# Kernel tuning notes

Measured on AMD Instinct MI355X. Metric: run time of the kernel, lower is better.

## Reference

```python
import jax, jax.numpy as jnp
import numpy as np


def setup_inputs() -> dict:
    key = jax.random.key(0)
    ks = jax.random.split(key, 9)
    n, L, H, H2 = 1024, 256, 512, 256
    return {
        "lstms0": jax.random.normal(ks[0], (n, L), jnp.float32),
        "lstms1": jax.random.normal(ks[1], (n, L), jnp.float32),
        "W_foh": jax.random.normal(ks[2], (2 * L, H), jnp.float32) * 0.05,
        "W_fom": jax.random.normal(ks[3], (2 * L, H), jnp.float32) * 0.05,
        "catBias": jax.random.normal(ks[4], (1, 2 * H), jnp.float32) * 0.05,
        "hid2Layer": jax.random.normal(ks[5], (2 * H, H2), jnp.float32) * 0.05,
        "hid2Bias": jax.random.normal(ks[6], (1, H2), jnp.float32) * 0.05,
        "outLayer": jax.random.normal(ks[7], (H2, 1), jnp.float32) * 0.05,
        "outBias": jax.random.normal(ks[8], (1, 1), jnp.float32) * 0.05,
    }


def reference(lstms0, lstms1, W_foh, W_fom, catBias, hid2Layer, hid2Bias, outLayer, outBias):
    act = jnp.tanh
    H = W_foh.shape[1]
    # per-token concatenated BiLSTM state: [n, 2L]
    x = jnp.concatenate([lstms0, lstms1], axis=-1)
    headfov = x @ W_foh  # [n, H]
    modfov = x @ W_fom   # [n, H]
    # activation(concat(head_i, mod_j) + catBias) is elementwise, so it splits:
    ah = act(headfov + catBias[0, :H])  # [n, H]
    am = act(modfov + catBias[0, H:])   # [n, H]
    # concat(ah_i, am_j) @ hid2Layer == ah_i @ W_top + am_j @ W_bot
    A = ah @ hid2Layer[:H]  # [n, H2]
    B = am @ hid2Layer[H:]  # [n, H2]
    # pairwise hidden: [n_head, n_mod, H2]
    Z = act(A[:, None, :] + B[None, :, :] + hid2Bias[0])
    scores = jnp.einsum("ijh,h->ij", Z, outLayer[:, 0]) + outBias[0, 0]
    return scores  # [n, n], scores[i, j] = score(head=i, mod=j)
```

## Files before the change

### kernel.cpp

```cpp
#include <hip/hip_runtime.h>
#include <hip/hip_bf16.h>

typedef short s16x8 __attribute__((ext_vector_type(8)));
typedef float f32x4 __attribute__((ext_vector_type(4)));

#define LOG2E_2 2.8853900817779268f

__device__ __forceinline__ float fexp2(float x){ return __builtin_amdgcn_exp2f(x); }
__device__ __forceinline__ float frcp (float x){ return __builtin_amdgcn_rcpf(x); }
__device__ __forceinline__ float ftanh(float v){
    return 1.0f - 2.0f * frcp(1.0f + fexp2(LOG2E_2 * v));
}
__device__ __forceinline__ unsigned short f2bf(float v){
    __hip_bfloat16 h = __float2bfloat16(v);
    return __builtin_bit_cast(unsigned short, h);
}
__device__ __forceinline__ float bf2f(unsigned short u){
    return __bfloat162float(__builtin_bit_cast(__hip_bfloat16, u));
}
__device__ __forceinline__ f32x4 mfma32(s16x8 a, s16x8 b, f32x4 c){
    return __builtin_amdgcn_mfma_f32_16x16x32_bf16(a, b, c, 0, 0, 0);
}

__global__ __launch_bounds__(256) void prep_all(
    const float* __restrict__ l0, const float* __restrict__ l1,
    const float* __restrict__ Wfoh, const float* __restrict__ Wfom,
    const float* __restrict__ W2,
    unsigned short* __restrict__ xhi, unsigned short* __restrict__ xlo,
    unsigned short* __restrict__ w1hi, unsigned short* __restrict__ w1lo,
    unsigned short* __restrict__ w2hi, unsigned short* __restrict__ w2lo)
{
    __shared__ float F[32][33];
    const int t = threadIdx.x;
    const int bid = blockIdx.x;

    if (bid < 512) {
        int idx = (bid * 256 + t) * 4;
        int r = idx >> 9, c = idx & 511;
        float4 v = (c < 256) ? *(const float4*)(l0 + r*256 + c)
                             : *(const float4*)(l1 + r*256 + (c - 256));
        ushort4 h, l;
        h.x = f2bf(v.x); l.x = f2bf(v.x - bf2f(h.x));
        h.y = f2bf(v.y); l.y = f2bf(v.y - bf2f(h.y));
        h.z = f2bf(v.z); l.z = f2bf(v.z - bf2f(h.z));
        h.w = f2bf(v.w); l.w = f2bf(v.w - bf2f(h.w));
        *(ushort4*)(xhi + idx) = h;
        *(ushort4*)(xlo + idx) = l;
        return;
    }

    const float* srcA; const float* srcB;
    int splitN, lda, K, k0, n0;
    unsigned short *dhi, *dlo;
    if (bid < 1024) {
        int b = bid - 512;
        k0 = (b & 15) * 32; n0 = (b >> 4) * 32;
        srcA = Wfoh; srcB = Wfom; splitN = 512; lda = 512; K = 512;
        dhi = w1hi; dlo = w1lo;
    } else {
        int b = bid - 1024;
        k0 = (b & 31) * 32; n0 = (b >> 5) * 32;
        srcA = W2; srcB = W2; splitN = 1 << 30; lda = 256; K = 1024;
        dhi = w2hi; dlo = w2lo;
    }
    {
        int kk = t >> 3, n4 = (t & 7) * 4;
        int n = n0 + n4;
        const float* s = (n < splitN) ? (srcA + (k0+kk)*lda + n)
                                      : (srcB + (k0+kk)*lda + (n - splitN));
        float4 v = *(const float4*)s;
        F[kk][n4+0] = v.x; F[kk][n4+1] = v.y; F[kk][n4+2] = v.z; F[kk][n4+3] = v.w;
    }
    __syncthreads();
    {
        int nn = t >> 3, k4 = (t & 7) * 4;
        ushort4 h, l;
        float v0 = F[k4+0][nn]; h.x = f2bf(v0); l.x = f2bf(v0 - bf2f(h.x));
        float v1 = F[k4+1][nn]; h.y = f2bf(v1); l.y = f2bf(v1 - bf2f(h.y));
        float v2 = F[k4+2][nn]; h.z = f2bf(v2); l.z = f2bf(v2 - bf2f(h.z));
        float v3 = F[k4+3][nn]; h.w = f2bf(v3); l.w = f2bf(v3 - bf2f(h.w));
        *(ushort4*)(dhi + (n0+nn)*K + k0 + k4) = h;
        *(ushort4*)(dlo + (n0+nn)*K + k0 + k4) = l;
    }
}

__global__ __launch_bounds__(256) void k1_mfma(
    const unsigned short* __restrict__ xhi, const unsigned short* __restrict__ xlo,
    const unsigned short* __restrict__ whi, const unsigned short* __restrict__ wlo,
    const float* __restrict__ cb,
    unsigned short* __restrict__ hvhi, unsigned short* __restrict__ hvlo)
{
    __shared__ unsigned short Ah[64][40], Al[64][40], Bh[32][40], Bl[32][40];
    const int t = threadIdx.x;
    const int r0 = blockIdx.y * 64, c0 = blockIdx.x * 32;
    const int w = t >> 6, lane = t & 63;
    const int m = lane & 15, quad = lane >> 4;

    const int arow = t >> 2, aseg = t & 3;
    const int brow = (t & 127) >> 2, bseg = t & 3;
    const bool doB = (t < 128);

    f32x4 acc0 = {0,0,0,0}, acc1 = {0,0,0,0};

    const unsigned short* pAh = xhi + (r0+arow)*512 + aseg*8;
    const unsigned short* pAl = xlo + (r0+arow)*512 + aseg*8;
    const unsigned short* pBh = whi + (c0+brow)*512 + bseg*8;
    const unsigned short* pBl = wlo + (c0+brow)*512 + bseg*8;

    uint4 pah = *(const uint4*)pAh;
    uint4 pal = *(const uint4*)pAl;
    uint4 pbh = {}, pbl = {};
    if (doB) { pbh = *(const uint4*)pBh; pbl = *(const uint4*)pBl; }

    for (int c = 0; c < 16; ++c) {
        __syncthreads();
        *(uint4*)&Ah[arow][aseg*8] = pah;
        *(uint4*)&Al[arow][aseg*8] = pal;
        if (doB) {
            *(uint4*)&Bh[brow][bseg*8] = pbh;
            *(uint4*)&Bl[brow][bseg*8] = pbl;
        }
        __syncthreads();
        if (c + 1 < 16) {
            int k0 = (c+1) * 32;
            pah = *(const uint4*)(pAh + k0);
            pal = *(const uint4*)(pAl + k0);
            if (doB) {
                pbh = *(const uint4*)(pBh + k0);
                pbl = *(const uint4*)(pBl + k0);
            }
        }
        {
            const int ko = quad*8;
            s16x8 ah  = *(const s16x8*)&Ah[w*16 + m][ko];
            s16x8 al  = *(const s16x8*)&Al[w*16 + m][ko];
            s16x8 b0h = *(const s16x8*)&Bh[m][ko];
            s16x8 b0l = *(const s16x8*)&Bl[m][ko];
            s16x8 b1h = *(const s16x8*)&Bh[16 + m][ko];
            s16x8 b1l = *(const s16x8*)&Bl[16 + m][ko];
            acc0 = mfma32(ah, b0h, acc0);
            acc0 = mfma32(ah, b0l, acc0);
            acc0 = mfma32(al, b0h, acc0);
            acc1 = mfma32(ah, b1h, acc1);
            acc1 = mfma32(ah, b1l, acc1);
            acc1 = mfma32(al, b1h, acc1);
        }
    }

    #pragma unroll
    for (int nt = 0; nt < 2; ++nt) {
        f32x4 a = nt ? acc1 : acc0;
        const int col = c0 + nt*16 + m;
        const float bias = cb[col];
        #pragma unroll
        for (int reg = 0; reg < 4; ++reg) {
            const int row = r0 + w*16 + quad*4 + reg;
            float v = ftanh(a[reg] + bias);
            unsigned short h = f2bf(v);
            unsigned short l = f2bf(v - bf2f(h));
            hvhi[row*1024 + col] = h;
            hvlo[row*1024 + col] = l;
        }
    }
}

__global__ __launch_bounds__(256) void k2_mfma(
    const unsigned short* __restrict__ hvhi, const unsigned short* __restrict__ hvlo,
    const unsigned short* __restrict__ w2hi, const unsigned short* __restrict__ w2lo,
    const float* __restrict__ h2b, float* __restrict__ P)
{
    __shared__ unsigned short Ah[64][40], Al[64][40], Bh[32][40], Bl[32][40];
    const int t = threadIdx.x;
    const int r0 = blockIdx.y * 64, c0 = blockIdx.x * 32;
    const int half = (c0 >= 256) ? 1 : 0;
    const int ho = half * 512;
    const int nw = c0 & 255;
    const int w = t >> 6, lane = t & 63;
    const int m = lane & 15, quad = lane >> 4;

    const int arow = t >> 2, aseg = t & 3;
    const int brow = (t & 127) >> 2, bseg = t & 3;
    const bool doB = (t < 128);

    f32x4 acc0 = {0,0,0,0}, acc1 = {0,0,0,0};

    const unsigned short* pAh = hvhi + (r0+arow)*1024 + ho + aseg*8;
    const unsigned short* pAl = hvlo + (r0+arow)*1024 + ho + aseg*8;
    const unsigned short* pBh = w2hi + (nw+brow)*1024 + ho + bseg*8;
    const unsigned short* pBl = w2lo + (nw+brow)*1024 + ho + bseg*8;

    uint4 pah = *(const uint4*)pAh;
    uint4 pal = *(const uint4*)pAl;
    uint4 pbh = {}, pbl = {};
    if (doB) { pbh = *(const uint4*)pBh; pbl = *(const uint4*)pBl; }

    for (int c = 0; c < 16; ++c) {
        __syncthreads();
        *(uint4*)&Ah[arow][aseg*8] = pah;
        *(uint4*)&Al[arow][aseg*8] = pal;
        if (doB) {
            *(uint4*)&Bh[brow][bseg*8] = pbh;
            *(uint4*)&Bl[brow][bseg*8] = pbl;
        }
        __syncthreads();
        if (c + 1 < 16) {
            int k0 = (c+1) * 32;
            pah = *(const uint4*)(pAh + k0);
            pal = *(const uint4*)(pAl + k0);
            if (doB) {
                pbh = *(const uint4*)(pBh + k0);
                pbl = *(const uint4*)(pBl + k0);
            }
        }
        {
            const int ko = quad*8;
            s16x8 ah  = *(const s16x8*)&Ah[w*16 + m][ko];
            s16x8 al  = *(const s16x8*)&Al[w*16 + m][ko];
            s16x8 b0h = *(const s16x8*)&Bh[m][ko];
            s16x8 b0l = *(const s16x8*)&Bl[m][ko];
            s16x8 b1h = *(const s16x8*)&Bh[16 + m][ko];
            s16x8 b1l = *(const s16x8*)&Bl[16 + m][ko];
            acc0 = mfma32(ah, b0h, acc0);
            acc0 = mfma32(ah, b0l, acc0);
            acc0 = mfma32(al, b0h, acc0);
            acc1 = mfma32(ah, b1h, acc1);
            acc1 = mfma32(ah, b1l, acc1);
            acc1 = mfma32(al, b1h, acc1);
        }
    }

    #pragma unroll
    for (int nt = 0; nt < 2; ++nt) {
        f32x4 a = nt ? acc1 : acc0;
        const int col = c0 + nt*16 + m;
        const float bias = half ? 0.0f : h2b[col];
        #pragma unroll
        for (int reg = 0; reg < 4; ++reg) {
            const int row = r0 + w*16 + quad*4 + reg;
            P[row*512 + col] = fexp2((a[reg] + bias) * LOG2E_2);
        }
    }
}

__global__ __launch_bounds__(256) void k3_pairwise(
    const float* __restrict__ P, const float* __restrict__ w,
    const float* __restrict__ ob, float* __restrict__ out)
{
    __shared__ float As[64][68];
    __shared__ float Bs[32][68];
    __shared__ float wls[256];
    const int tid = threadIdx.x;
    const int tx = tid & 15;
    const int ty = tid >> 4;
    const int i0 = blockIdx.y * 64, j0 = blockIdx.x * 32;

    wls[tid] = w[tid];

    const int ar = tid >> 2, ac = (tid & 3) * 16;
    const int br = tid >> 3, bc = (tid & 7) * 8;

    const float* pA = P + (i0 + ar) * 512 + ac;
    const float* pB = P + (j0 + br) * 512 + 256 + bc;

    float acc[4][2] = {};
    float4 ra[4], rb[2];
    #pragma unroll
    for (int k = 0; k < 4; ++k) ra[k] = *(const float4*)(pA + k*4);
    #pragma unroll
    for (int k = 0; k < 2; ++k) rb[k] = *(const float4*)(pB + k*4);

    for (int c = 0; c < 4; ++c) {
        __syncthreads();
        #pragma unroll
        for (int k = 0; k < 4; ++k) *(float4*)&As[ar][ac + k*4] = ra[k];
        #pragma unroll
        for (int k = 0; k < 2; ++k) *(float4*)&Bs[br][bc + k*4] = rb[k];
        __syncthreads();
        if (c + 1 < 4) {
            int off = (c + 1) * 64;
            #pragma unroll
            for (int k = 0; k < 4; ++k) ra[k] = *(const float4*)(pA + off + k*4);
            #pragma unroll
            for (int k = 0; k < 2; ++k) rb[k] = *(const float4*)(pB + off + k*4);
        }

        #pragma unroll 2
        for (int hh = 0; hh < 64; hh += 4) {
            float4 wv = *(const float4*)&wls[c*64 + hh];
            float4 av[4];
            #pragma unroll
            for (int r = 0; r < 4; ++r) av[r] = *(const float4*)&As[ty*4 + r][hh];
            float4 bv[2];
            #pragma unroll
            for (int q = 0; q < 2; ++q) bv[q] = *(const float4*)&Bs[tx + 16*q][hh];
            #pragma unroll
            for (int r = 0; r < 4; ++r)
                #pragma unroll
                for (int q = 0; q < 2; ++q) {
                    float u0 = fmaf(av[r].x, bv[q].x, 1.0f);
                    float u1 = fmaf(av[r].y, bv[q].y, 1.0f);
                    float u2 = fmaf(av[r].z, bv[q].z, 1.0f);
                    float u3 = fmaf(av[r].w, bv[q].w, 1.0f);
                    float d01 = u0 * u1;
                    float d23 = u2 * u3;
                    float p01 = fmaf(wv.x, u1, wv.y * u0);
                    float p23 = fmaf(wv.z, u3, wv.w * u2);
                    float num = fmaf(p01, d23, p23 * d01);
                    acc[r][q] = fmaf(num, frcp(d01 * d23), acc[r][q]);
                }
        }
    }

    float sumw = 0.0f;
    #pragma unroll
    for (int h = 0; h < 256; h += 4) {
        float4 wv = *(const float4*)&wls[h];
        sumw += (wv.x + wv.y) + (wv.z + wv.w);
    }
    const float base = ob[0] + sumw;
    #pragma unroll
    for (int r = 0; r < 4; ++r) {
        const int row = i0 + ty*4 + r;
        out[row*1024 + j0 + tx]      = base - 2.0f * acc[r][0];
        out[row*1024 + j0 + tx + 16] = base - 2.0f * acc[r][1];
    }
}

extern "C" void kernel_launch(void* const* d_in, const int* in_sizes, int n_in,
                              void* d_out, int out_size, void* d_ws, size_t ws_size,
                              hipStream_t stream) {
    const float* l0   = (const float*)d_in[0];
    const float* l1   = (const float*)d_in[1];
    const float* Wfoh = (const float*)d_in[2];
    const float* Wfom = (const float*)d_in[3];
    const float* cb   = (const float*)d_in[4];
    const float* W2   = (const float*)d_in[5];
    const float* h2b  = (const float*)d_in[6];
    const float* w    = (const float*)d_in[7];
    const float* ob   = (const float*)d_in[8];
    float* out = (float*)d_out;

    unsigned short* hv_hi  = (unsigned short*)d_ws;
    unsigned short* hv_lo  = hv_hi + 1024*1024;
    float*          P      = (float*)(hv_lo + 1024*1024);
    unsigned short* xs_hi  = (unsigned short*)(P + 1024*512);
    unsigned short* xs_lo  = xs_hi + 1024*512;
    unsigned short* w1t_hi = xs_lo + 1024*512;
    unsigned short* w1t_lo = w1t_hi + 1024*512;
    unsigned short* w2t_hi = w1t_lo + 1024*512;
    unsigned short* w2t_lo = w2t_hi + 256*1024;

    prep_all<<<1280, 256, 0, stream>>>(l0, l1, Wfoh, Wfom, W2,
                                       xs_hi, xs_lo, w1t_hi, w1t_lo, w2t_hi, w2t_lo);
    k1_mfma<<<dim3(32,16), 256, 0, stream>>>(xs_hi, xs_lo, w1t_hi, w1t_lo, cb, hv_hi, hv_lo);
    k2_mfma<<<dim3(16,16), 256, 0, stream>>>(hv_hi, hv_lo, w2t_hi, w2t_lo, h2b, P);
    k3_pairwise<<<dim3(32,16), 256, 0, stream>>>(P, w, ob, out);
}
```

Before: 129.1 us.

## Double-buffer LDS tiles in GEMM kernels and shrink pairwise tile to 32x32

```diff
diff --git a/kernel.cpp b/kernel.cpp
--- a/kernel.cpp
+++ b/kernel.cpp
@@ -90,7 +90,7 @@
     const float* __restrict__ cb,
     unsigned short* __restrict__ hvhi, unsigned short* __restrict__ hvlo)
 {
-    __shared__ unsigned short Ah[64][40], Al[64][40], Bh[32][40], Bl[32][40];
+    __shared__ unsigned short Ah[2][64][40], Al[2][64][40], Bh[2][32][40], Bl[2][32][40];
     const int t = threadIdx.x;
     const int r0 = blockIdx.y * 64, c0 = blockIdx.x * 32;
     const int w = t >> 6, lane = t & 63;
@@ -112,38 +112,50 @@
     uint4 pbh = {}, pbl = {};
     if (doB) { pbh = *(const uint4*)pBh; pbl = *(const uint4*)pBl; }
 
+    *(uint4*)&Ah[0][arow][aseg*8] = pah;
+    *(uint4*)&Al[0][arow][aseg*8] = pal;
+    if (doB) {
+        *(uint4*)&Bh[0][brow][bseg*8] = pbh;
+        *(uint4*)&Bl[0][brow][bseg*8] = pbl;
+    }
+    pah = *(const uint4*)(pAh + 32);
+    pal = *(const uint4*)(pAl + 32);
+    if (doB) { pbh = *(const uint4*)(pBh + 32); pbl = *(const uint4*)(pBl + 32); }
+    __syncthreads();
+
+    #pragma unroll 2
     for (int c = 0; c < 16; ++c) {
-        __syncthreads();
-        *(uint4*)&Ah[arow][aseg*8] = pah;
-        *(uint4*)&Al[arow][aseg*8] = pal;
-        if (doB) {
-            *(uint4*)&Bh[brow][bseg*8] = pbh;
-            *(uint4*)&Bl[brow][bseg*8] = pbl;
-        }
-        __syncthreads();
-        if (c + 1 < 16) {
-            int k0 = (c+1) * 32;
-            pah = *(const uint4*)(pAh + k0);
-            pal = *(const uint4*)(pAl + k0);
-            if (doB) {
-                pbh = *(const uint4*)(pBh + k0);
-                pbl = *(const uint4*)(pBl + k0);
-            }
-        }
+        const int buf = c & 1;
         {
             const int ko = quad*8;
-            s16x8 ah  = *(const s16x8*)&Ah[w*16 + m][ko];
-            s16x8 al  = *(const s16x8*)&Al[w*16 + m][ko];
-            s16x8 b0h = *(const s16x8*)&Bh[m][ko];
-            s16x8 b0l = *(const s16x8*)&Bl[m][ko];
-            s16x8 b1h = *(const s16x8*)&Bh[16 + m][ko];
-            s16x8 b1l = *(const s16x8*)&Bl[16 + m][ko];
+            s16x8 ah  = *(const s16x8*)&Ah[buf][w*16 + m][ko];
+            s16x8 al  = *(const s16x8*)&Al[buf][w*16 + m][ko];
+            s16x8 b0h = *(const s16x8*)&Bh[buf][m][ko];
+            s16x8 b0l = *(const s16x8*)&Bl[buf][m][ko];
+            s16x8 b1h = *(const s16x8*)&Bh[buf][16 + m][ko];
+            s16x8 b1l = *(const s16x8*)&Bl[buf][16 + m][ko];
             acc0 = mfma32(ah, b0h, acc0);
             acc0 = mfma32(ah, b0l, acc0);
             acc0 = mfma32(al, b0h, acc0);
             acc1 = mfma32(ah, b1h, acc1);
             acc1 = mfma32(ah, b1l, acc1);
             acc1 = mfma32(al, b1h, acc1);
+        }
+        if (c + 1 < 16) {
+            const int nb = buf ^ 1;
+            *(uint4*)&Ah[nb][arow][aseg*8] = pah;
+            *(uint4*)&Al[nb][arow][aseg*8] = pal;
+            if (doB) {
+                *(uint4*)&Bh[nb][brow][bseg*8] = pbh;
+                *(uint4*)&Bl[nb][brow][bseg*8] = pbl;
+            }
+            if (c + 2 < 16) {
+                const int k0 = (c+2) * 32;
+                pah = *(const uint4*)(pAh + k0);
+                pal = *(const uint4*)(pAl + k0);
+                if (doB) { pbh = *(const uint4*)(pBh + k0); pbl = *(const uint4*)(pBl + k0); }
+            }
+            __syncthreads();
         }
     }
 
@@ -169,7 +181,7 @@
     const unsigned short* __restrict__ w2hi, const unsigned short* __restrict__ w2lo,
     const float* __restrict__ h2b, float* __restrict__ P)
 {
-    __shared__ unsigned short Ah[64][40], Al[64][40], Bh[32][40], Bl[32][40];
+    __shared__ unsigned short Ah[2][64][40], Al[2][64][40], Bh[2][32][40], Bl[2][32][40];
     const int t = threadIdx.x;
     const int r0 = blockIdx.y * 64, c0 = blockIdx.x * 32;
     const int half = (c0 >= 256) ? 1 : 0;
@@ -194,38 +206,50 @@
     uint4 pbh = {}, pbl = {};
     if (doB) { pbh = *(const uint4*)pBh; pbl = *(const uint4*)pBl; }
 
+    *(uint4*)&Ah[0][arow][aseg*8] = pah;
+    *(uint4*)&Al[0][arow][aseg*8] = pal;
+    if (doB) {
+        *(uint4*)&Bh[0][brow][bseg*8] = pbh;
+        *(uint4*)&Bl[0][brow][bseg*8] = pbl;
+    }
+    pah = *(const uint4*)(pAh + 32);
+    pal = *(const uint4*)(pAl + 32);
+    if (doB) { pbh = *(const uint4*)(pBh + 32); pbl = *(const uint4*)(pBl + 32); }
+    __syncthreads();
+
+    #pragma unroll 2
     for (int c = 0; c < 16; ++c) {
-        __syncthreads();
-        *(uint4*)&Ah[arow][aseg*8] = pah;
-        *(uint4*)&Al[arow][aseg*8] = pal;
-        if (doB) {
-            *(uint4*)&Bh[brow][bseg*8] = pbh;
-            *(uint4*)&Bl[brow][bseg*8] = pbl;
-        }
-        __syncthreads();
-        if (c + 1 < 16) {
-            int k0 = (c+1) * 32;
-            pah = *(const uint4*)(pAh + k0);
-            pal = *(const uint4*)(pAl + k0);
-            if (doB) {
-                pbh = *(const uint4*)(pBh + k0);
-                pbl = *(const uint4*)(pBl + k0);
-            }
-        }
+        const int buf = c & 1;
         {
             const int ko = quad*8;
-            s16x8 ah  = *(const s16x8*)&Ah[w*16 + m][ko];
-            s16x8 al  = *(const s16x8*)&Al[w*16 + m][ko];
-            s16x8 b0h = *(const s16x8*)&Bh[m][ko];
-            s16x8 b0l = *(const s16x8*)&Bl[m][ko];
-            s16x8 b1h = *(const s16x8*)&Bh[16 + m][ko];
-            s16x8 b1l = *(const s16x8*)&Bl[16 + m][ko];
+            s16x8 ah  = *(const s16x8*)&Ah[buf][w*16 + m][ko];
+            s16x8 al  = *(const s16x8*)&Al[buf][w*16 + m][ko];
+            s16x8 b0h = *(const s16x8*)&Bh[buf][m][ko];
+            s16x8 b0l = *(const s16x8*)&Bl[buf][m][ko];
+            s16x8 b1h = *(const s16x8*)&Bh[buf][16 + m][ko];
+            s16x8 b1l = *(const s16x8*)&Bl[buf][16 + m][ko];
             acc0 = mfma32(ah, b0h, acc0);
             acc0 = mfma32(ah, b0l, acc0);
             acc0 = mfma32(al, b0h, acc0);
             acc1 = mfma32(ah, b1h, acc1);
             acc1 = mfma32(ah, b1l, acc1);
             acc1 = mfma32(al, b1h, acc1);
+        }
+        if (c + 1 < 16) {
+            const int nb = buf ^ 1;
+            *(uint4*)&Ah[nb][arow][aseg*8] = pah;
+            *(uint4*)&Al[nb][arow][aseg*8] = pal;
+            if (doB) {
+                *(uint4*)&Bh[nb][brow][bseg*8] = pbh;
+                *(uint4*)&Bl[nb][brow][bseg*8] = pbl;
+            }
+            if (c + 2 < 16) {
+                const int k0 = (c+2) * 32;
+                pah = *(const uint4*)(pAh + k0);
+                pal = *(const uint4*)(pAl + k0);
+                if (doB) { pbh = *(const uint4*)(pBh + k0); pbl = *(const uint4*)(pBl + k0); }
+            }
+            __syncthreads();
         }
     }
 
@@ -246,55 +270,51 @@
     const float* __restrict__ P, const float* __restrict__ w,
     const float* __restrict__ ob, float* __restrict__ out)
 {
-    __shared__ float As[64][68];
-    __shared__ float Bs[32][68];
+    __shared__ float As[2][32][68];
+    __shared__ float Bs[2][32][68];
     __shared__ float wls[256];
     const int tid = threadIdx.x;
     const int tx = tid & 15;
     const int ty = tid >> 4;
-    const int i0 = blockIdx.y * 64, j0 = blockIdx.x * 32;
+    const int i0 = blockIdx.y * 32, j0 = blockIdx.x * 32;
 
     wls[tid] = w[tid];
 
-    const int ar = tid >> 2, ac = (tid & 3) * 16;
-    const int br = tid >> 3, bc = (tid & 7) * 8;
+    const int ar = tid >> 3, ac = (tid & 7) * 8;
 
     const float* pA = P + (i0 + ar) * 512 + ac;
-    const float* pB = P + (j0 + br) * 512 + 256 + bc;
-
-    float acc[4][2] = {};
-    float4 ra[4], rb[2];
-    #pragma unroll
-    for (int k = 0; k < 4; ++k) ra[k] = *(const float4*)(pA + k*4);
-    #pragma unroll
-    for (int k = 0; k < 2; ++k) rb[k] = *(const float4*)(pB + k*4);
-
+    const float* pB = P + (j0 + ar) * 512 + 256 + ac;
+
+    float4 ra0 = *(const float4*)(pA);
+    float4 ra1 = *(const float4*)(pA + 4);
+    float4 rb0 = *(const float4*)(pB);
+    float4 rb1 = *(const float4*)(pB + 4);
+
+    *(float4*)&As[0][ar][ac]   = ra0;
+    *(float4*)&As[0][ar][ac+4] = ra1;
+    *(float4*)&Bs[0][ar][ac]   = rb0;
+    *(float4*)&Bs[0][ar][ac+4] = rb1;
+    ra0 = *(const float4*)(pA + 64);
+    ra1 = *(const float4*)(pA + 68);
+    rb0 = *(const float4*)(pB + 64);
+    rb1 = *(const float4*)(pB + 68);
+    __syncthreads();
+
+    float acc[2][2] = {};
+
+    #pragma unroll 2
     for (int c = 0; c < 4; ++c) {
-        __syncthreads();
-        #pragma unroll
-        for (int k = 0; k < 4; ++k) *(float4*)&As[ar][ac + k*4] = ra[k];
-        #pragma unroll
-        for (int k = 0; k < 2; ++k) *(float4*)&Bs[br][bc + k*4] = rb[k];
-        __syncthreads();
-        if (c + 1 < 4) {
-            int off = (c + 1) * 64;
-            #pragma unroll
-            for (int k = 0; k < 4; ++k) ra[k] = *(const float4*)(pA + off + k*4);
-            #pragma unroll
-            for (int k = 0; k < 2; ++k) rb[k] = *(const float4*)(pB + off + k*4);
-        }
-
-        #pragma unroll 2
+        const int buf = c & 1;
+        #pragma unroll 4
         for (int hh = 0; hh < 64; hh += 4) {
             float4 wv = *(const float4*)&wls[c*64 + hh];
-            float4 av[4];
+            float4 av[2], bv[2];
+            av[0] = *(const float4*)&As[buf][ty][hh];
+            av[1] = *(const float4*)&As[buf][ty+16][hh];
+            bv[0] = *(const float4*)&Bs[buf][tx][hh];
+            bv[1] = *(const float4*)&Bs[buf][tx+16][hh];
             #pragma unroll
-            for (int r = 0; r < 4; ++r) av[r] = *(const float4*)&As[ty*4 + r][hh];
-            float4 bv[2];
-            #pragma unroll
-            for (int q = 0; q < 2; ++q) bv[q] = *(const float4*)&Bs[tx + 16*q][hh];
-            #pragma unroll
-            for (int r = 0; r < 4; ++r)
+            for (int r = 0; r < 2; ++r)
                 #pragma unroll
                 for (int q = 0; q < 2; ++q) {
                     float u0 = fmaf(av[r].x, bv[q].x, 1.0f);
@@ -309,6 +329,21 @@
                     acc[r][q] = fmaf(num, frcp(d01 * d23), acc[r][q]);
                 }
         }
+        if (c + 1 < 4) {
+            const int nb = buf ^ 1;
+            *(float4*)&As[nb][ar][ac]   = ra0;
+            *(float4*)&As[nb][ar][ac+4] = ra1;
+            *(float4*)&Bs[nb][ar][ac]   = rb0;
+            *(float4*)&Bs[nb][ar][ac+4] = rb1;
+            if (c + 2 < 4) {
+                const int off = (c + 2) * 64;
+                ra0 = *(const float4*)(pA + off);
+                ra1 = *(const float4*)(pA + off + 4);
+                rb0 = *(const float4*)(pB + off);
+                rb1 = *(const float4*)(pB + off + 4);
+            }
+            __syncthreads();
+        }
     }
 
     float sumw = 0.0f;
@@ -318,12 +353,10 @@
         sumw += (wv.x + wv.y) + (wv.z + wv.w);
     }
     const float base = ob[0] + sumw;
-    #pragma unroll
-    for (int r = 0; r < 4; ++r) {
-        const int row = i0 + ty*4 + r;
-        out[row*1024 + j0 + tx]      = base - 2.0f * acc[r][0];
-        out[row*1024 + j0 + tx + 16] = base - 2.0f * acc[r][1];
-    }
+    out[(i0+ty)*1024    + j0+tx]      = base - 2.0f * acc[0][0];
+    out[(i0+ty)*1024    + j0+tx+16]   = base - 2.0f * acc[0][1];
+    out[(i0+ty+16)*1024 + j0+tx]      = base - 2.0f * acc[1][0];
+    out[(i0+ty+16)*1024 + j0+tx+16]   = base - 2.0f * acc[1][1];
 }
 
 extern "C" void kernel_launch(void* const* d_in, const int* in_sizes, int n_in,
@@ -354,5 +387,5 @@
                                        xs_hi, xs_lo, w1t_hi, w1t_lo, w2t_hi, w2t_lo);
     k1_mfma<<<dim3(32,16), 256, 0, stream>>>(xs_hi, xs_lo, w1t_hi, w1t_lo, cb, hv_hi, hv_lo);
     k2_mfma<<<dim3(16,16), 256, 0, stream>>>(hv_hi, hv_lo, w2t_hi, w2t_lo, h2b, P);
-    k3_pairwise<<<dim3(32,16), 256, 0, stream>>>(P, w, ob, out);
-}
+    k3_pairwise<<<dim3(32,32), 256, 0, stream>>>(P, w, ob, out);
+}
```

Result: faster. 123.3 us (-4.5%).
